# Performance work log

Measured on AMD Instinct MI355X. Metric: run time of the kernel, lower is better.

## Reference

```python
import jax, jax.numpy as jnp
import numpy as np

T = 131072      # sequence length (time steps)
IN = 256        # input_dim (MAX_NEURAL_UNITS)
G = 8           # num_dataset_groups
H = 64          # ssm_io_dim (== ssm_dim)
CTX = 8         # context_dim
P = 32          # complex state size = ssm_dim // 2 (conj_sym=True)
NL = 4          # ssm_num_layers
OUT = 2         # output_dim
DT_MIN, DT_MAX = 1e-3, 1e-1


def setup_inputs() -> dict:
    ks = jax.random.split(jax.random.key(0), 16)
    n = lambda i, shape, s=1.0: jax.random.normal(ks[i], shape, dtype=jnp.float32) * s
    return {
        "x": n(0, (T, IN)),
        "group_idx": 3,
        "enc_w": n(1, (G, H - CTX, IN), 1.0 / np.sqrt(IN)),
        "enc_b": n(2, (G, H - CTX), 0.01),
        "ctx_emb": n(3, (G, CTX)),
        "Lambda_re": -0.5 * jnp.abs(n(4, (NL, P))) - 0.1,   # stable (negative real part)
        "Lambda_im": n(5, (NL, P)) * 3.0,
        "B_re": n(6, (NL, P, H), 1.0 / np.sqrt(H)),
        "B_im": n(7, (NL, P, H), 1.0 / np.sqrt(H)),
        "C_re": n(8, (NL, H, P), 1.0 / np.sqrt(P)),
        "C_im": n(9, (NL, H, P), 1.0 / np.sqrt(P)),
        "D": n(10, (NL, H)),
        "log_step": jax.random.uniform(ks[11], (NL, P), jnp.float32, np.log(DT_MIN), np.log(DT_MAX)),
        "norm_scale": jnp.ones((NL, H), jnp.float32),
        "norm_bias": jnp.zeros((NL, H), jnp.float32),
        "glu_w1": n(12, (NL, H, H), 1.0 / np.sqrt(H)),
        "glu_b1": jnp.zeros((NL, H), jnp.float32),
        "glu_w2": n(13, (NL, H, H), 1.0 / np.sqrt(H)),
        "glu_b2": jnp.zeros((NL, H), jnp.float32),
        "dec_w": n(14, (OUT, H), 1.0 / np.sqrt(H)),
        "dec_b": jnp.zeros((OUT,), jnp.float32),
    }


def _s5_scan(Lbar, Bu):
    """Linear recurrence x_k = Lbar * x_{k-1} + Bu_k via parallel associative scan."""
    A = jnp.broadcast_to(Lbar, Bu.shape)  # (T, P) complex

    def binop(a, b):
        a1, u1 = a
        a2, u2 = b
        return a2 * a1, a2 * u1 + u2

    _, xs = jax.lax.associative_scan(binop, (A, Bu))
    return xs  # (T, P) complex


def reference(x, group_idx, enc_w, enc_b, ctx_emb, Lambda_re, Lambda_im, B_re, B_im,
              C_re, C_im, D, log_step, norm_scale, norm_bias,
              glu_w1, glu_b1, glu_w2, glu_b2, dec_w, dec_b):
    # group-routed encoder (lax.switch over per-group Linears == gather of weights)
    h = x @ enc_w[group_idx].T + enc_b[group_idx]                         # (T, H-CTX)
    ctx = jnp.broadcast_to(ctx_emb[group_idx], (h.shape[0], CTX))         # (T, CTX)
    h = jnp.concatenate([h, ctx], axis=1)                                 # (T, H)

    for i in range(NL):  # static layer stack
        skip = h
        # batch-norm over the time axis (training-mode batch statistics)
        mu = jnp.mean(h, axis=0)
        var = jnp.var(h, axis=0)
        hn = (h - mu) * jax.lax.rsqrt(var + 1e-5) * norm_scale[i] + norm_bias[i]

        # ZOH discretisation of diagonal complex SSM
        Lam = jax.lax.complex(Lambda_re[i], Lambda_im[i])                 # (P,)
        dt = jnp.exp(log_step[i])                                         # (P,) step_rescale=1
        Lbar = jnp.exp(Lam * dt)                                          # (P,)
        Bt = jax.lax.complex(B_re[i], B_im[i])                            # (P, H)
        Bbar = (((Lbar - 1.0) / Lam)[:, None]) * Bt                       # (P, H)

        Bu = hn.astype(Bbar.dtype) @ Bbar.T                               # (T, P) complex
        xs = _s5_scan(Lbar, Bu)                                           # (T, P)
        Cm = jax.lax.complex(C_re[i], C_im[i])                            # (H, P)
        y = 2.0 * jnp.real(xs @ Cm.T) + hn * D[i]                         # conj_sym output

        # half-GLU nonlinearity + residual (dropout inactive at inference)
        y = jax.nn.gelu(y)
        y = (y @ glu_w1[i].T + glu_b1[i]) * jax.nn.sigmoid(y @ glu_w2[i].T + glu_b2[i])
        h = skip + y

    return h @ dec_w.T + dec_b                                            # (T, OUT)
```

## Files before the change

kernel.cpp:

```cpp
#include <hip/hip_runtime.h>

#define T_LEN   131072
#define IN_DIM  256
#define HD      64
#define PD      32
#define NLAY    4
#define CHUNK   128
#define NBLK    (T_LEN / CHUNK)
#define ASTR    68

typedef __attribute__((ext_vector_type(8))) short bf16x8;
typedef __attribute__((ext_vector_type(4))) float f32x4;

union FragU { uint4 q; bf16x8 v; };

__device__ __forceinline__ unsigned splitpack(float x) {
    unsigned xb = __float_as_uint(x);
    unsigned hb = (xb + 0x8000u) & 0xffff0000u;
    float lf = x - __uint_as_float(hb);
    unsigned lb = (__float_as_uint(lf) + 0x8000u) >> 16;
    return (hb >> 16) | (lb << 16);
}

__device__ __forceinline__ void packAB(float4 a0, float4 a1, bf16x8& hi, bf16x8& lo) {
    unsigned p0 = splitpack(a0.x), p1 = splitpack(a0.y);
    unsigned p2 = splitpack(a0.z), p3 = splitpack(a0.w);
    unsigned p4 = splitpack(a1.x), p5 = splitpack(a1.y);
    unsigned p6 = splitpack(a1.z), p7 = splitpack(a1.w);
    union { bf16x8 v; unsigned u[4]; } H, L;
    H.u[0] = (p0 & 0xffffu) | (p1 << 16);
    H.u[1] = (p2 & 0xffffu) | (p3 << 16);
    H.u[2] = (p4 & 0xffffu) | (p5 << 16);
    H.u[3] = (p6 & 0xffffu) | (p7 << 16);
    L.u[0] = (p0 >> 16) | (p1 & 0xffff0000u);
    L.u[1] = (p2 >> 16) | (p3 & 0xffff0000u);
    L.u[2] = (p4 >> 16) | (p5 & 0xffff0000u);
    L.u[3] = (p6 >> 16) | (p7 & 0xffff0000u);
    hi = H.v; lo = L.v;
}

#define MFMA3(ACC, AH, AL, BH, BL)                                              \
    ACC = __builtin_amdgcn_mfma_f32_16x16x32_bf16(AH, BH, ACC, 0, 0, 0);        \
    ACC = __builtin_amdgcn_mfma_f32_16x16x32_bf16(AH, BL, ACC, 0, 0, 0);        \
    ACC = __builtin_amdgcn_mfma_f32_16x16x32_bf16(AL, BH, ACC, 0, 0, 0);

__device__ __forceinline__ int kmap(int q, int j) {
    return (j < 4) ? (q * 4 + j) : (16 + q * 4 + (j - 4));
}

__global__ __launch_bounds__(512) void ssm_k0a(
    const float* __restrict__ Lre, const float* __restrict__ Lim,
    const float* __restrict__ logstep,
    float* __restrict__ Lbar, float* __restrict__ Ldt, float* __restrict__ stats)
{
    int tid = threadIdx.x;
    if (tid < NLAY * PD) {
        int l = tid >> 5, p = tid & 31;
        float dt = expf(logstep[l * PD + p]);
        float lr = Lre[l * PD + p], li = Lim[l * PD + p];
        float ldr = lr * dt, ldi = li * dt;
        Ldt[tid * 2] = ldr; Ldt[tid * 2 + 1] = ldi;
        float e = expf(ldr);
        float sn, cs; sincosf(ldi, &sn, &cs);
        Lbar[tid * 2] = e * cs; Lbar[tid * 2 + 1] = e * sn;
    }
    if (tid < NLAY * 128) stats[tid] = 0.0f;
}

__global__ __launch_bounds__(256) void ssm_k0b(
    const float* __restrict__ Lre, const float* __restrict__ Lim,
    const float* __restrict__ logstep,
    const float* __restrict__ Bre, const float* __restrict__ Bim,
    const float* __restrict__ Cre, const float* __restrict__ Cim,
    const float* __restrict__ w1, const float* __restrict__ w2,
    const float* __restrict__ enc_w, const int* __restrict__ gptr,
    unsigned* __restrict__ fragE, unsigned* __restrict__ fragL)
{
    int fi = blockIdx.x * 256 + threadIdx.x;
    if (fi >= 10240) return;
    int g = gptr[0];
    int mat, lay = 0, rem;
    unsigned* outp;
    if (fi < 2048) { mat = 0; rem = fi; outp = fragE + rem * 8; }
    else {
        int t = fi - 2048;
        lay = t / 2048;
        int r2 = t % 2048;
        mat = 1 + r2 / 512;
        rem = r2 % 512;
        outp = fragL + ((size_t)(lay * 4 + (mat - 1)) * 512 + rem) * 8;
    }
    int ks = rem / 256;
    int nt = (rem / 64) & 3;
    int lane = rem & 63;
    int q = lane >> 4;
    int n = nt * 16 + (lane & 15);

    float vals[8];
#pragma unroll
    for (int j = 0; j < 8; ++j) {
        int k = ks * 32 + kmap(q, j);
        float v;
        if (mat == 0) {
            v = (n < 56) ? enc_w[(size_t)(g * 56 + n) * IN_DIM + k] : 0.0f;
        } else if (mat == 1) {
            int p = n >> 1;
            float dt = expf(logstep[lay * PD + p]);
            float lr = Lre[lay * PD + p], li = Lim[lay * PD + p];
            float e = expf(lr * dt);
            float sn, cs; sincosf(li * dt, &sn, &cs);
            float den = lr * lr + li * li;
            float nr = e * cs - 1.0f, ni = e * sn;
            float fr = (nr * lr + ni * li) / den, fimag = (ni * lr - nr * li) / den;
            float br = Bre[(lay * PD + p) * HD + k], bi = Bim[(lay * PD + p) * HD + k];
            v = (n & 1) ? (fr * bi + fimag * br) : (fr * br - fimag * bi);
        } else if (mat == 2) {
            int p = k >> 1;
            v = (k & 1) ? -Cim[((size_t)lay * HD + n) * PD + p]
                        :  Cre[((size_t)lay * HD + n) * PD + p];
        } else if (mat == 3) {
            v = w1[((size_t)lay * HD + n) * HD + k];
        } else {
            v = w2[((size_t)lay * HD + n) * HD + k];
        }
        vals[j] = v;
    }
    unsigned p8[8];
#pragma unroll
    for (int j = 0; j < 8; ++j) p8[j] = splitpack(vals[j]);
#pragma unroll
    for (int w = 0; w < 4; ++w) {
        unsigned p0 = p8[2 * w], p1 = p8[2 * w + 1];
        outp[w]     = (p0 & 0xffffu) | (p1 << 16);
        outp[4 + w] = (p0 >> 16) | (p1 & 0xffff0000u);
    }
}

__global__ __launch_bounds__(64) void ssm_k5_reduce(
    const float* __restrict__ part, float* __restrict__ statsL)
{
    int c = blockIdx.x;
    int lane = threadIdx.x;
    float s = 0.0f;
#pragma unroll
    for (int j = 0; j < 4; ++j) {
        float4 v = *(const float4*)&part[c * 1024 + j * 256 + lane * 4];
        s += v.x + v.y + v.z + v.w;
    }
#pragma unroll
    for (int m = 1; m < 64; m <<= 1) s += __shfl_xor(s, m, 64);
    if (lane == 0) statsL[c] = s;
}

__global__ __launch_bounds__(512, 4) void ssm_k1_encoder(
    const float* __restrict__ x, const int* __restrict__ gptr,
    const unsigned* __restrict__ fragE, const float* __restrict__ enc_b,
    const float* __restrict__ ctx_emb,
    float* __restrict__ h, float* __restrict__ part)
{
    __shared__ float sp1[512], sp2[512];
    int tid = threadIdx.x;
    int l = tid & 63, w = tid >> 6;
    int cq = l >> 4, cr = l & 15;
    int g = gptr[0];
    size_t r0 = (size_t)blockIdx.x * 128;
    int arow = 16 * w + cr;
    const float* xrow = &x[(r0 + arow) * IN_DIM];
    const f32x4 fzero = {0.f, 0.f, 0.f, 0.f};

    float4 cur[16];
#pragma unroll
    for (int kt = 0; kt < 4; ++kt)
#pragma unroll
        for (int ks = 0; ks < 2; ++ks) {
            cur[kt * 4 + 2 * ks]     = *(const float4*)&xrow[kt * 64 + ks * 32 + cq * 4];
            cur[kt * 4 + 2 * ks + 1] = *(const float4*)&xrow[kt * 64 + ks * 32 + cq * 4 + 16];
        }

    f32x4 acc[4];
#pragma unroll
    for (int nt = 0; nt < 4; ++nt) acc[nt] = fzero;

#pragma unroll
    for (int kt = 0; kt < 4; ++kt)
#pragma unroll
        for (int ks = 0; ks < 2; ++ks) {
            bf16x8 ah, al;
            packAB(cur[kt * 4 + 2 * ks], cur[kt * 4 + 2 * ks + 1], ah, al);
            int ksg = kt * 2 + ks;
#pragma unroll
            for (int nt = 0; nt < 4; ++nt) {
                const uint4* wf = (const uint4*)&fragE[((size_t)(ksg * 4 + nt) * 64 + l) * 8];
                FragU BH, BL; BH.q = wf[0]; BL.q = wf[1];
                MFMA3(acc[nt], ah, al, BH.v, BL.v);
            }
        }
#pragma unroll
    for (int nt = 0; nt < 4; ++nt) {
        int ch = nt * 16 + cr;
        float eb = (ch < 56) ? enc_b[g * 56 + ch] : 0.0f;
        bool isctx = (ch >= 56);
        float cv = isctx ? ctx_emb[g * 8 + (ch - 56)] : 0.0f;
        float v1 = 0.0f, v2 = 0.0f;
#pragma unroll
        for (int r = 0; r < 4; ++r) {
            float val = isctx ? cv : (acc[nt][r] + eb);
            h[(r0 + 16 * w + 4 * cq + r) * HD + ch] = val;
            v1 += val; v2 += val * val;
        }
        v1 += __shfl_xor(v1, 16, 64); v2 += __shfl_xor(v2, 16, 64);
        v1 += __shfl_xor(v1, 32, 64); v2 += __shfl_xor(v2, 32, 64);
        if (l < 16) { sp1[w * 64 + ch] = v1; sp2[w * 64 + ch] = v2; }
    }
    __syncthreads();
    if (tid < 64) {
        float s1 = 0.0f, s2 = 0.0f;
#pragma unroll
        for (int ww = 0; ww < 8; ++ww) { s1 += sp1[ww * 64 + tid]; s2 += sp2[ww * 64 + tid]; }
        part[tid * 1024 + blockIdx.x]        = s1;
        part[(64 + tid) * 1024 + blockIdx.x] = s2;
    }
}

__global__ __launch_bounds__(512, 4) void ssm_k2_bu_scan(
    const float* __restrict__ h, const float* __restrict__ stats,
    const float* __restrict__ nscale, const float* __restrict__ nbias,
    const unsigned* __restrict__ fragL, const float* __restrict__ Lbar,
    float* __restrict__ xs, float* __restrict__ carry, int lay)
{
    __shared__ __attribute__((aligned(16))) float bf[128 * ASTR];
    __shared__ float lsa[HD], lsb[HD];
    int tid = threadIdx.x;
    int l = tid & 63, w = tid >> 6;
    int cq = l >> 4, cr = l & 15;
    size_t r0 = (size_t)blockIdx.x * CHUNK;
    int arow = 16 * w + cr;
    const f32x4 fzero = {0.f, 0.f, 0.f, 0.f};

    if (tid < HD) {
        float s1 = stats[lay * 128 + tid], s2 = stats[lay * 128 + 64 + tid];
        float mu = s1 * (1.0f / T_LEN);
        float var = fmaxf(s2 * (1.0f / T_LEN) - mu * mu, 0.0f);
        float sc = nscale[lay * HD + tid] * rsqrtf(var + 1e-5f);
        lsa[tid] = sc;
        lsb[tid] = nbias[lay * HD + tid] - mu * sc;
    }
    __syncthreads();

    const float* hrowp = &h[(r0 + arow) * HD];
    const unsigned* fB = fragL + (size_t)(lay * 4 + 0) * 4096;
    f32x4 acc[4];
#pragma unroll
    for (int nt = 0; nt < 4; ++nt) acc[nt] = fzero;
#pragma unroll
    for (int ks = 0; ks < 2; ++ks) {
        int k0 = ks * 32 + cq * 4;
        float4 c0 = *(const float4*)&hrowp[k0];
        float4 c1 = *(const float4*)&hrowp[k0 + 16];
        c0.x = c0.x * lsa[k0]      + lsb[k0];
        c0.y = c0.y * lsa[k0 + 1]  + lsb[k0 + 1];
        c0.z = c0.z * lsa[k0 + 2]  + lsb[k0 + 2];
        c0.w = c0.w * lsa[k0 + 3]  + lsb[k0 + 3];
        c1.x = c1.x * lsa[k0 + 16] + lsb[k0 + 16];
        c1.y = c1.y * lsa[k0 + 17] + lsb[k0 + 17];
        c1.z = c1.z * lsa[k0 + 18] + lsb[k0 + 18];
        c1.w = c1.w * lsa[k0 + 19] + lsb[k0 + 19];
        bf16x8 ah, al;
        packAB(c0, c1, ah, al);
#pragma unroll
        for (int nt = 0; nt < 4; ++nt) {
            const uint4* wf = (const uint4*)&fB[((size_t)(ks * 4 + nt) * 64 + l) * 8];
            FragU BH, BL; BH.q = wf[0]; BL.q = wf[1];
            MFMA3(acc[nt], ah, al, BH.v, BL.v);
        }
    }
#pragma unroll
    for (int nt = 0; nt < 4; ++nt)
#pragma unroll
        for (int r = 0; r < 4; ++r)
            bf[(16 * w + 4 * cq + r) * ASTR + nt * 16 + cr] = acc[nt][r];
    __syncthreads();

    if (tid < 64) {
        int p = l >> 1;
        float Lr = Lbar[(lay * PD + p) * 2];
        float Lj = Lbar[(lay * PD + p) * 2 + 1];
        float csn = (l & 1) ? Lj : -Lj;
        float xv = 0.0f;
        for (int t = 0; t < CHUNK; ++t) {
            float b = bf[t * ASTR + l];
            float xo = __shfl_xor(xv, 1, 64);
            xv = Lr * xv + csn * xo + b;
            bf[t * ASTR + l] = xv;
        }
        carry[(size_t)blockIdx.x * 64 + l] = xv;
    }
    __syncthreads();
#pragma unroll
    for (int j = 0; j < 4; ++j) {
        float4 v = *(float4*)&bf[arow * ASTR + cq * 16 + j * 4];
        *(float4*)&xs[(r0 + arow) * HD + cq * 16 + j * 4] = v;
    }
}

__global__ __launch_bounds__(64) void ssm_k3_carry(
    const float* __restrict__ carry, const float* __restrict__ Ldt,
    float* __restrict__ pc, int lay)
{
    int p = blockIdx.x;
    int lane = threadIdx.x;
    float ldr = Ldt[(lay * PD + p) * 2], ldi = Ldt[(lay * PD + p) * 2 + 1];
    float er = __expf(ldr * (float)CHUNK);
    float an = ldi * (float)CHUNK;
    float lcr = er * __cosf(an), lci = er * __sinf(an);
    float cr[16], ci[16];
#pragma unroll
    for (int j = 0; j < 16; ++j) {
        cr[j] = carry[(size_t)(lane * 16 + j) * 64 + 2 * p];
        ci[j] = carry[(size_t)(lane * 16 + j) * 64 + 2 * p + 1];
    }
    float ur = 0.0f, ui = 0.0f;
#pragma unroll
    for (int j = 0; j < 16; ++j) {
        float nr = lcr * ur - lci * ui + cr[j];
        float ni = lcr * ui + lci * ur + ci[j];
        ur = nr; ui = ni;
    }
    float mr = lcr, mi = lci;
#pragma unroll
    for (int s = 0; s < 4; ++s) { float t = mr * mr - mi * mi; mi = 2.0f * mr * mi; mr = t; }
#pragma unroll
    for (int d = 1; d < 64; d <<= 1) {
        float tr = __shfl_up(ur, d, 64);
        float ti = __shfl_up(ui, d, 64);
        if (lane >= d) { ur = mr * tr - mi * ti + ur; ui = mr * ti + mi * tr + ui; }
        float t = mr * mr - mi * mi; mi = 2.0f * mr * mi; mr = t;
    }
    float pr = __shfl_up(ur, 1, 64), pi = __shfl_up(ui, 1, 64);
    float xr = (lane == 0) ? 0.0f : pr;
    float xi = (lane == 0) ? 0.0f : pi;
#pragma unroll
    for (int j = 0; j < 16; ++j) {
        pc[(size_t)(lane * 16 + j) * 64 + 2 * p]     = xr;
        pc[(size_t)(lane * 16 + j) * 64 + 2 * p + 1] = xi;
        float nr = lcr * xr - lci * xi + cr[j];
        float ni = lcr * xi + lci * xr + ci[j];
        xr = nr; xi = ni;
    }
}

template <bool LAST>
__global__ __launch_bounds__(512, 4) void ssm_k4_out(
    const float* __restrict__ h, const float* __restrict__ xs,
    const float* __restrict__ pc, const float* __restrict__ stats,
    const float* __restrict__ nscale, const float* __restrict__ nbias,
    const float* __restrict__ Ldt, const unsigned* __restrict__ fragL,
    const float* __restrict__ Dv,
    const float* __restrict__ b1, const float* __restrict__ b2,
    float* __restrict__ hout, float* __restrict__ part,
    const float* __restrict__ dec_w, const float* __restrict__ dec_b,
    float* __restrict__ outp, int lay)
{
    __shared__ __attribute__((aligned(16))) unsigned act[128 * ASTR];
    __shared__ float lsa[HD], lsb[HD], lsd[HD], lpc[HD], lld[HD];
    __shared__ float sp1[512], sp2[512];
    int tid = threadIdx.x;
    int l = tid & 63, w = tid >> 6;
    int cq = l >> 4, cr = l & 15;
    size_t r0 = (size_t)blockIdx.x * CHUNK;
    int arow = 16 * w + cr;
    const f32x4 fzero = {0.f, 0.f, 0.f, 0.f};

    if (tid < HD) {
        float s1 = stats[lay * 128 + tid], s2 = stats[lay * 128 + 64 + tid];
        float mu = s1 * (1.0f / T_LEN);
        float var = fmaxf(s2 * (1.0f / T_LEN) - mu * mu, 0.0f);
        float sc = nscale[lay * HD + tid] * rsqrtf(var + 1e-5f);
        lsa[tid] = sc;
        lsb[tid] = nbias[lay * HD + tid] - mu * sc;
        lsd[tid] = Dv[lay * HD + tid];
        lpc[tid] = pc[(size_t)blockIdx.x * 64 + tid];
        lld[tid] = Ldt[lay * 64 + tid];
    }
    __syncthreads();

    const unsigned* fC = fragL + (size_t)(lay * 4 + 1) * 4096;
    f32x4 yacc[4];
#pragma unroll
    for (int nt = 0; nt < 4; ++nt) yacc[nt] = fzero;
    {
        const float* xrowp = &xs[(r0 + arow) * HD];
        float tt = (float)(arow + 1);
#pragma unroll
        for (int ks = 0; ks < 2; ++ks) {
            int k0 = ks * 32 + cq * 4;
            float4 v0 = *(const float4*)&xrowp[k0];
            float4 v1 = *(const float4*)&xrowp[k0 + 16];
            {
                float e1 = __expf(lld[k0] * tt), an = lld[k0 + 1] * tt;
                float prr = e1 * __cosf(an), pri = e1 * __sinf(an);
                v0.x += prr * lpc[k0] - pri * lpc[k0 + 1];
                v0.y += prr * lpc[k0 + 1] + pri * lpc[k0];
            }
            {
                float e1 = __expf(lld[k0 + 2] * tt), an = lld[k0 + 3] * tt;
                float prr = e1 * __cosf(an), pri = e1 * __sinf(an);
                v0.z += prr * lpc[k0 + 2] - pri * lpc[k0 + 3];
                v0.w += prr * lpc[k0 + 3] + pri * lpc[k0 + 2];
            }
            {
                float e1 = __expf(lld[k0 + 16] * tt), an = lld[k0 + 17] * tt;
                float prr = e1 * __cosf(an), pri = e1 * __sinf(an);
                v1.x += prr * lpc[k0 + 16] - pri * lpc[k0 + 17];
                v1.y += prr * lpc[k0 + 17] + pri * lpc[k0 + 16];
            }
            {
                float e1 = __expf(lld[k0 + 18] * tt), an = lld[k0 + 19] * tt;
                float prr = e1 * __cosf(an), pri = e1 * __sinf(an);
                v1.z += prr * lpc[k0 + 18] - pri * lpc[k0 + 19];
                v1.w += prr * lpc[k0 + 19] + pri * lpc[k0 + 18];
            }
            bf16x8 ah, al;
            packAB(v0, v1, ah, al);
#pragma unroll
            for (int nt = 0; nt < 4; ++nt) {
                const uint4* wf = (const uint4*)&fC[((size_t)(ks * 4 + nt) * 64 + l) * 8];
                FragU BH, BL; BH.q = wf[0]; BL.q = wf[1];
                MFMA3(yacc[nt], ah, al, BH.v, BL.v);
            }
        }
    }

    float hrow[16];
#pragma unroll
    for (int nt = 0; nt < 4; ++nt) {
        int ch = nt * 16 + cr;
        float sav = lsa[ch], sbv = lsb[ch], dvv = lsd[ch];
#pragma unroll
        for (int r = 0; r < 4; ++r) {
            int row = 16 * w + 4 * cq + r;
            float hv = h[(r0 + row) * HD + ch];
            hrow[nt * 4 + r] = hv;
            float t = 2.0f * yacc[nt][r] + (hv * sav + sbv) * dvv;
            float u2 = 1.5957691216057308f * (t + 0.044715f * t * t * t);
            float gv = t / (1.0f + __expf(-u2));
            act[row * ASTR + ch] = splitpack(gv);
        }
    }
    asm volatile("s_waitcnt lgkmcnt(0)" ::: "memory");

    const unsigned* f1 = fragL + (size_t)(lay * 4 + 2) * 4096;
    const unsigned* f2 = fragL + (size_t)(lay * 4 + 3) * 4096;
    f32x4 uacc[4], sacc[4];
#pragma unroll
    for (int nt = 0; nt < 4; ++nt) { uacc[nt] = fzero; sacc[nt] = fzero; }
#pragma unroll
    for (int ks = 0; ks < 2; ++ks) {
        int col = ks * 32 + 4 * cq;
        uint4 a0 = *(const uint4*)&act[arow * ASTR + col];
        uint4 a1 = *(const uint4*)&act[arow * ASTR + col + 16];
        union { bf16x8 v; unsigned u[4]; } H, L;
        H.u[0] = (a0.x & 0xffffu) | (a0.y << 16);
        H.u[1] = (a0.z & 0xffffu) | (a0.w << 16);
        H.u[2] = (a1.x & 0xffffu) | (a1.y << 16);
        H.u[3] = (a1.z & 0xffffu) | (a1.w << 16);
        L.u[0] = (a0.x >> 16) | (a0.y & 0xffff0000u);
        L.u[1] = (a0.z >> 16) | (a0.w & 0xffff0000u);
        L.u[2] = (a1.x >> 16) | (a1.y & 0xffff0000u);
        L.u[3] = (a1.z >> 16) | (a1.w & 0xffff0000u);
#pragma unroll
        for (int nt = 0; nt < 4; ++nt) {
            const uint4* w1f = (const uint4*)&f1[((size_t)(ks * 4 + nt) * 64 + l) * 8];
            FragU BH1, BL1; BH1.q = w1f[0]; BL1.q = w1f[1];
            MFMA3(uacc[nt], H.v, L.v, BH1.v, BL1.v);
            const uint4* w2f = (const uint4*)&f2[((size_t)(ks * 4 + nt) * 64 + l) * 8];
            FragU BH2, BL2; BH2.q = w2f[0]; BL2.q = w2f[1];
            MFMA3(sacc[nt], H.v, L.v, BH2.v, BL2.v);
        }
    }

    if (LAST) {
        float o0[4] = {0.f, 0.f, 0.f, 0.f}, o1[4] = {0.f, 0.f, 0.f, 0.f};
#pragma unroll
        for (int nt = 0; nt < 4; ++nt) {
            int ch = nt * 16 + cr;
            float bb1 = b1[lay * HD + ch], bb2 = b2[lay * HD + ch];
            float dw0 = dec_w[ch], dw1 = dec_w[64 + ch];
#pragma unroll
            for (int r = 0; r < 4; ++r) {
                float sv = sacc[nt][r] + bb2;
                float sg = 1.0f / (1.0f + __expf(-sv));
                float ho = hrow[nt * 4 + r] + (uacc[nt][r] + bb1) * sg;
                o0[r] += ho * dw0;
                o1[r] += ho * dw1;
            }
        }
#pragma unroll
        for (int r = 0; r < 4; ++r) {
#pragma unroll
            for (int m = 1; m < 16; m <<= 1) {
                o0[r] += __shfl_xor(o0[r], m, 64);
                o1[r] += __shfl_xor(o1[r], m, 64);
            }
        }
        if (cr == 0) {
            float db0 = dec_b[0], db1 = dec_b[1];
#pragma unroll
            for (int r = 0; r < 4; ++r) {
                int row = 16 * w + 4 * cq + r;
                *(float2*)&outp[(r0 + row) * 2] = make_float2(o0[r] + db0, o1[r] + db1);
            }
        }
    } else {
#pragma unroll
        for (int nt = 0; nt < 4; ++nt) {
            int ch = nt * 16 + cr;
            float bb1 = b1[lay * HD + ch], bb2 = b2[lay * HD + ch];
            float v1 = 0.0f, v2 = 0.0f;
#pragma unroll
            for (int r = 0; r < 4; ++r) {
                int row = 16 * w + 4 * cq + r;
                float sv = sacc[nt][r] + bb2;
                float sg = 1.0f / (1.0f + __expf(-sv));
                float ho = hrow[nt * 4 + r] + (uacc[nt][r] + bb1) * sg;
                hout[(r0 + row) * HD + ch] = ho;
                v1 += ho; v2 += ho * ho;
            }
            v1 += __shfl_xor(v1, 16, 64); v2 += __shfl_xor(v2, 16, 64);
            v1 += __shfl_xor(v1, 32, 64); v2 += __shfl_xor(v2, 32, 64);
            if (l < 16) { sp1[w * 64 + ch] = v1; sp2[w * 64 + ch] = v2; }
        }
        __syncthreads();
        if (tid < 64) {
            float s1 = 0.0f, s2 = 0.0f;
#pragma unroll
            for (int ww = 0; ww < 8; ++ww) { s1 += sp1[ww * 64 + tid]; s2 += sp2[ww * 64 + tid]; }
            part[tid * 1024 + blockIdx.x]        = s1;
            part[(64 + tid) * 1024 + blockIdx.x] = s2;
        }
    }
}

extern "C" void kernel_launch(void* const* d_in, const int* in_sizes, int n_in,
                              void* d_out, int out_size, void* d_ws, size_t ws_size,
                              hipStream_t stream)
{
    (void)in_sizes; (void)n_in; (void)out_size; (void)ws_size;
    const float* x     = (const float*)d_in[0];
    const int*   gidx  = (const int*)d_in[1];
    const float* enc_w = (const float*)d_in[2];
    const float* enc_b = (const float*)d_in[3];
    const float* ctx   = (const float*)d_in[4];
    const float* Lre   = (const float*)d_in[5];
    const float* Lim   = (const float*)d_in[6];
    const float* Bre   = (const float*)d_in[7];
    const float* Bim   = (const float*)d_in[8];
    const float* Cre   = (const float*)d_in[9];
    const float* Cim   = (const float*)d_in[10];
    const float* Dv    = (const float*)d_in[11];
    const float* lstep = (const float*)d_in[12];
    const float* nsc   = (const float*)d_in[13];
    const float* nbi   = (const float*)d_in[14];
    const float* w1    = (const float*)d_in[15];
    const float* b1    = (const float*)d_in[16];
    const float* w2    = (const float*)d_in[17];
    const float* b2    = (const float*)d_in[18];
    const float* dw    = (const float*)d_in[19];
    const float* db    = (const float*)d_in[20];
    float* out = (float*)d_out;

    float* ws = (float*)d_ws;
    float* h     = ws;  ws += (size_t)T_LEN * HD;
    float* xs    = ws;  ws += (size_t)T_LEN * HD;
    float* carry = ws;  ws += (size_t)NBLK * HD;
    float* pc    = ws;  ws += (size_t)NBLK * HD;
    float* stats = ws;  ws += NLAY * 128;
    float* Lbar  = ws;  ws += NLAY * PD * 2;
    float* Ldt   = ws;  ws += NLAY * PD * 2;
    unsigned* fragE = (unsigned*)ws;  ws += 16384;
    unsigned* fragL = (unsigned*)ws;  ws += 65536;
    float* part  = ws;  ws += 128 * 1024;

    ssm_k0a<<<1, 512, 0, stream>>>(Lre, Lim, lstep, Lbar, Ldt, stats);
    ssm_k0b<<<40, 256, 0, stream>>>(Lre, Lim, lstep, Bre, Bim, Cre, Cim, w1, w2,
                                    enc_w, gidx, fragE, fragL);
    ssm_k1_encoder<<<1024, 512, 0, stream>>>(x, gidx, fragE, enc_b, ctx, h, part);
    ssm_k5_reduce<<<128, 64, 0, stream>>>(part, stats);
    for (int lay = 0; lay < NLAY; ++lay) {
        ssm_k2_bu_scan<<<NBLK, 512, 0, stream>>>(h, stats, nsc, nbi, fragL, Lbar, xs, carry, lay);
        ssm_k3_carry<<<PD, 64, 0, stream>>>(carry, Ldt, pc, lay);
        if (lay < NLAY - 1) {
            ssm_k4_out<false><<<NBLK, 512, 0, stream>>>(
                h, xs, pc, stats, nsc, nbi, Ldt, fragL, Dv, b1, b2,
                h, part, dw, db, out, lay);
            ssm_k5_reduce<<<128, 64, 0, stream>>>(part, stats + (lay + 1) * 128);
        } else {
            ssm_k4_out<true><<<NBLK, 512, 0, stream>>>(
                h, xs, pc, stats, nsc, nbi, Ldt, fragL, Dv, b1, b2,
                h, part, dw, db, out, lay);
        }
    }
}
```

Before: 326.3 us.

## Parallelise in-block scan across all waves and store xs as bf16

The intra-chunk linear recurrence, previously run serially over 128 steps by a single wave, is now split into eight 16-step segments, one per wave. Wave 0 combines the segment aggregates using Lbar^16, and the other waves then add the propagated prefix to their segments. Separately, the xs intermediate is written and read as bf16 instead of fp32, halving that buffer's memory traffic. The bf16 storage lowers the precision of the scan state before the C projection, which may increase error.

```diff
diff --git a/kernel.cpp b/kernel.cpp
--- a/kernel.cpp
+++ b/kernel.cpp
@@ -226,10 +226,12 @@
     const float* __restrict__ h, const float* __restrict__ stats,
     const float* __restrict__ nscale, const float* __restrict__ nbias,
     const unsigned* __restrict__ fragL, const float* __restrict__ Lbar,
-    float* __restrict__ xs, float* __restrict__ carry, int lay)
+    const float* __restrict__ Ldt,
+    unsigned short* __restrict__ xs, float* __restrict__ carry, int lay)
 {
     __shared__ __attribute__((aligned(16))) float bf[128 * ASTR];
-    __shared__ float lsa[HD], lsb[HD];
+    __shared__ float lsa[HD], lsb[HD], lld[HD];
+    __shared__ float agg[8 * 64], pref[8 * 64];
     int tid = threadIdx.x;
     int l = tid & 63, w = tid >> 6;
     int cq = l >> 4, cr = l & 15;
@@ -244,6 +246,7 @@
         float sc = nscale[lay * HD + tid] * rsqrtf(var + 1e-5f);
         lsa[tid] = sc;
         lsb[tid] = nbias[lay * HD + tid] - mu * sc;
+        lld[tid] = Ldt[lay * 64 + tid];
     }
     __syncthreads();
 
@@ -281,25 +284,72 @@
             bf[(16 * w + 4 * cq + r) * ASTR + nt * 16 + cr] = acc[nt][r];
     __syncthreads();
 
-    if (tid < 64) {
+    {
         int p = l >> 1;
         float Lr = Lbar[(lay * PD + p) * 2];
         float Lj = Lbar[(lay * PD + p) * 2 + 1];
         float csn = (l & 1) ? Lj : -Lj;
         float xv = 0.0f;
-        for (int t = 0; t < CHUNK; ++t) {
-            float b = bf[t * ASTR + l];
+        int t0 = 16 * w;
+#pragma unroll
+        for (int tl = 0; tl < 16; ++tl) {
+            float b = bf[(t0 + tl) * ASTR + l];
             float xo = __shfl_xor(xv, 1, 64);
             xv = Lr * xv + csn * xo + b;
-            bf[t * ASTR + l] = xv;
-        }
-        carry[(size_t)blockIdx.x * 64 + l] = xv;
+            bf[(t0 + tl) * ASTR + l] = xv;
+        }
+        agg[w * 64 + l] = xv;
     }
     __syncthreads();
-#pragma unroll
-    for (int j = 0; j < 4; ++j) {
-        float4 v = *(float4*)&bf[arow * ASTR + cq * 16 + j * 4];
-        *(float4*)&xs[(r0 + arow) * HD + cq * 16 + j * 4] = v;
+    if (w == 0) {
+        int p = l >> 1;
+        float ldr = lld[2 * p], ldi = lld[2 * p + 1];
+        float e16 = __expf(ldr * 16.0f);
+        float an = ldi * 16.0f;
+        float lcr = e16 * __cosf(an), lci = e16 * __sinf(an);
+        float csn16 = (l & 1) ? lci : -lci;
+        float pv = 0.0f;
+#pragma unroll
+        for (int ww = 0; ww < 8; ++ww) {
+            pref[ww * 64 + l] = pv;
+            float a = agg[ww * 64 + l];
+            float po = __shfl_xor(pv, 1, 64);
+            pv = lcr * pv + csn16 * po + a;
+        }
+        carry[(size_t)blockIdx.x * 64 + l] = pv;
+    }
+    __syncthreads();
+    if (w > 0) {
+        int p = l >> 1;
+        float Lr = Lbar[(lay * PD + p) * 2];
+        float Li = Lbar[(lay * PD + p) * 2 + 1];
+        float P  = pref[w * 64 + l];
+        float Po = __shfl_xor(P, 1, 64);
+        float mr = Lr, mi = Li;
+        int t0 = 16 * w;
+#pragma unroll
+        for (int tl = 0; tl < 16; ++tl) {
+            float msn = (l & 1) ? mi : -mi;
+            bf[(t0 + tl) * ASTR + l] += mr * P + msn * Po;
+            float nmr = mr * Lr - mi * Li;
+            float nmi = mr * Li + mi * Lr;
+            mr = nmr; mi = nmi;
+        }
+    }
+    __syncthreads();
+#pragma unroll
+    for (int j = 0; j < 2; ++j) {
+        unsigned uu[4];
+#pragma unroll
+        for (int q2 = 0; q2 < 4; ++q2) {
+            float a = bf[arow * ASTR + cq * 16 + j * 8 + q2 * 2];
+            float b = bf[arow * ASTR + cq * 16 + j * 8 + q2 * 2 + 1];
+            unsigned ua = (__float_as_uint(a) + 0x8000u) >> 16;
+            unsigned ub = (__float_as_uint(b) + 0x8000u) & 0xffff0000u;
+            uu[q2] = ua | ub;
+        }
+        *(uint4*)&xs[(r0 + arow) * HD + cq * 16 + j * 8] =
+            make_uint4(uu[0], uu[1], uu[2], uu[3]);
     }
 }
 
@@ -351,7 +401,7 @@
 
 template <bool LAST>
 __global__ __launch_bounds__(512, 4) void ssm_k4_out(
-    const float* __restrict__ h, const float* __restrict__ xs,
+    const float* __restrict__ h, const unsigned short* __restrict__ xs,
     const float* __restrict__ pc, const float* __restrict__ stats,
     const float* __restrict__ nscale, const float* __restrict__ nbias,
     const float* __restrict__ Ldt, const unsigned* __restrict__ fragL,
@@ -389,13 +439,19 @@
 #pragma unroll
     for (int nt = 0; nt < 4; ++nt) yacc[nt] = fzero;
     {
-        const float* xrowp = &xs[(r0 + arow) * HD];
+        const unsigned short* xrowp = &xs[(r0 + arow) * HD];
         float tt = (float)(arow + 1);
 #pragma unroll
         for (int ks = 0; ks < 2; ++ks) {
             int k0 = ks * 32 + cq * 4;
-            float4 v0 = *(const float4*)&xrowp[k0];
-            float4 v1 = *(const float4*)&xrowp[k0 + 16];
+            uint2 q0 = *(const uint2*)&xrowp[k0];
+            uint2 q1 = *(const uint2*)&xrowp[k0 + 16];
+            float4 v0 = make_float4(
+                __uint_as_float(q0.x << 16), __uint_as_float(q0.x & 0xffff0000u),
+                __uint_as_float(q0.y << 16), __uint_as_float(q0.y & 0xffff0000u));
+            float4 v1 = make_float4(
+                __uint_as_float(q1.x << 16), __uint_as_float(q1.x & 0xffff0000u),
+                __uint_as_float(q1.y << 16), __uint_as_float(q1.y & 0xffff0000u));
             {
                 float e1 = __expf(lld[k0] * tt), an = lld[k0 + 1] * tt;
                 float prr = e1 * __cosf(an), pri = e1 * __sinf(an);
@@ -571,7 +627,7 @@
 
     float* ws = (float*)d_ws;
     float* h     = ws;  ws += (size_t)T_LEN * HD;
-    float* xs    = ws;  ws += (size_t)T_LEN * HD;
+    unsigned short* xs = (unsigned short*)ws;  ws += (size_t)T_LEN * HD / 2;
     float* carry = ws;  ws += (size_t)NBLK * HD;
     float* pc    = ws;  ws += (size_t)NBLK * HD;
     float* stats = ws;  ws += NLAY * 128;
@@ -587,7 +643,8 @@
     ssm_k1_encoder<<<1024, 512, 0, stream>>>(x, gidx, fragE, enc_b, ctx, h, part);
     ssm_k5_reduce<<<128, 64, 0, stream>>>(part, stats);
     for (int lay = 0; lay < NLAY; ++lay) {
-        ssm_k2_bu_scan<<<NBLK, 512, 0, stream>>>(h, stats, nsc, nbi, fragL, Lbar, xs, carry, lay);
+        ssm_k2_bu_scan<<<NBLK, 512, 0, stream>>>(h, stats, nsc, nbi, fragL, Lbar, Ldt,
+                                                 xs, carry, lay);
         ssm_k3_carry<<<PD, 64, 0, stream>>>(carry, Ldt, pc, lay);
         if (lay < NLAY - 1) {
             ssm_k4_out<false><<<NBLK, 512, 0, stream>>>(
```

After: 271.6 us. 1.2x faster.
